# Optimization experiments

Measured on AMD Instinct MI355X. Metric: run time of the kernel, lower is better.

## Reference

```python
import jax, jax.numpy as jnp
import numpy as np

N = 50000      # nodes
E = 640000     # edges
D = 128        # input_dim
O = 128        # output_dim
R = 8          # num_rels


def _uniform(k, shape, fan_in):
    s = 1.0 / np.sqrt(fan_in)
    return jax.random.uniform(k, shape, jnp.float32, -s, s)


def setup_inputs() -> dict:
    key = jax.random.key(0)
    ks = jax.random.split(key, 12)
    x = jax.random.normal(ks[0], (N, D), jnp.float32)
    src = jax.random.randint(ks[1], (E,), 0, N, jnp.int32)
    dst = jax.random.randint(ks[2], (E,), 0, N, jnp.int32)
    etype = jax.random.randint(ks[3], (E,), 0, R, jnp.int32)
    # TypedLinear relation weight bank [R, D, O]
    W_rel = _uniform(ks[4], (R, D, O), D)
    # w1: Linear(D, D)
    w1_W = _uniform(ks[5], (D, D), D)
    w1_b = _uniform(ks[6], (D,), D)
    # MLP (2 layers): Linear(D, O) -> relu -> Linear(O, O)
    m1_W = _uniform(ks[7], (D, O), D)
    m1_b = _uniform(ks[8], (O,), D)
    m2_W = _uniform(ks[9], (O, O), O)
    m2_b = _uniform(ks[10], (O,), O)
    return {"x": x, "src": src, "dst": dst, "etype": etype,
            "W_rel": W_rel, "w1_W": w1_W, "w1_b": w1_b,
            "m1_W": m1_W, "m1_b": m1_b, "m2_W": m2_W, "m2_b": m2_b}


def reference(x, src, dst, etype, W_rel, w1_W, w1_b, m1_W, m1_b, m2_W, m2_b):
    # TypedLinear message: m_e = x[src_e] @ W_rel[etype_e]
    # Since R is small, precompute all relation projections per node [N, R, O]
    # then gather per edge -- avoids materializing per-edge [E, D, O] weights.
    h_all = jnp.einsum('nd,rdo->nro', x, W_rel)          # [N, R, O]
    m = h_all[src, etype]                                 # [E, O] gather
    # scatter-sum aggregation into destination nodes
    agg = jax.ops.segment_sum(m, dst, num_segments=x.shape[0])  # [N, O]
    # update: w1(feat_in) + inneigh, then MLP (linear-relu-linear)
    h = x @ w1_W + w1_b + agg
    h = jax.nn.relu(h @ m1_W + m1_b)
    return h @ m2_W + m2_b
```

## Files before the change

### kernel.cpp

```cpp
#include <hip/hip_runtime.h>
#include <hip/hip_bf16.h>
#include <stdint.h>

#define N_NODES 50000
#define E_EDGES 640000
#define NB_TILES 782
#define NKEY 400000
#define NKEYP 400384
#define SCAN_BLOCKS 391

typedef __attribute__((ext_vector_type(8))) short short8;
typedef __attribute__((ext_vector_type(4))) float float4v;

__device__ __forceinline__ unsigned short f32_to_bf16(float f) {
  uint32_t u = __float_as_uint(f);
  u += 0x7fffu + ((u >> 16) & 1u);
  return (unsigned short)(u >> 16);
}
__device__ __forceinline__ float bf16_to_f32(unsigned short h) {
  return __uint_as_float(((uint32_t)h) << 16);
}

__global__ __launch_bounds__(256) void k_pre(
    const float* __restrict__ x, const float* __restrict__ W_rel,
    const float* __restrict__ w1W, const float* __restrict__ m1W,
    const float* __restrict__ m2W, const int* __restrict__ dst,
    const int* __restrict__ ety,
    unsigned short* __restrict__ xb, unsigned short* __restrict__ wTg,
    int* __restrict__ cnt) {
  int b = blockIdx.x;
  if (b < 6250) {
    int idx = b * 256 + threadIdx.x;
    float4 v = ((const float4*)x)[idx];
    uint32_t p0 = (uint32_t)f32_to_bf16(v.x) | ((uint32_t)f32_to_bf16(v.y) << 16);
    uint32_t p1 = (uint32_t)f32_to_bf16(v.z) | ((uint32_t)f32_to_bf16(v.w) << 16);
    ((uint2*)xb)[idx] = make_uint2(p0, p1);
  } else if (b < 6261) {
    int m = b - 6250;
    const float* srcp = (m < 8) ? (W_rel + (size_t)m * 16384)
                                : (m == 8 ? w1W : (m == 9 ? m1W : m2W));
    unsigned short* dstp = wTg + (size_t)m * 16384;
    for (int i = 0; i < 64; ++i) {
      int idx = threadIdx.x + i * 256;
      int o = idx >> 7, k = idx & 127;
      dstp[idx] = f32_to_bf16(srcp[k * 128 + o]);
    }
  } else {
    int e = (b - 6261) * 256 + threadIdx.x;
    atomicAdd(&cnt[dst[e] * 8 + ety[e]], 1);
  }
}

__global__ __launch_bounds__(1024) void k_scanA(
    const int* __restrict__ cnt, int* __restrict__ off, int* __restrict__ btot) {
  __shared__ int s[1024];
  int t = threadIdx.x, g = blockIdx.x * 1024 + t;
  int v = cnt[g];
  s[t] = v; __syncthreads();
  for (int d = 1; d < 1024; d <<= 1) {
    int a = (t >= d) ? s[t - d] : 0;
    __syncthreads();
    s[t] += a;
    __syncthreads();
  }
  off[g] = s[t] - v;
  if (t == 1023) btot[blockIdx.x] = s[t];
}

__global__ __launch_bounds__(512) void k_scanB(int* __restrict__ btot) {
  __shared__ int s[512];
  int t = threadIdx.x;
  int v = (t < SCAN_BLOCKS) ? btot[t] : 0;
  s[t] = v; __syncthreads();
  for (int d = 1; d < 512; d <<= 1) {
    int a = (t >= d) ? s[t - d] : 0;
    __syncthreads();
    s[t] += a;
    __syncthreads();
  }
  if (t < SCAN_BLOCKS) btot[t] = s[t] - v;
}

__global__ __launch_bounds__(1024) void k_scanC(
    int* __restrict__ off, const int* __restrict__ btot) {
  int g = blockIdx.x * 1024 + threadIdx.x;
  off[g] += btot[blockIdx.x];
}

__global__ __launch_bounds__(256) void k_fill(
    const int* __restrict__ src, const int* __restrict__ dst,
    const int* __restrict__ ety, int* __restrict__ off,
    int* __restrict__ eidx) {
  int e = blockIdx.x * 256 + threadIdx.x;
  if (e >= E_EDGES) return;
  int key = dst[e] * 8 + ety[e];
  int p = atomicAdd(&off[key], 1);
  eidx[p] = src[e];
}

__device__ __forceinline__ void gemm_tile_g(const short (*A)[136],
    const unsigned short* __restrict__ Bt, int wave, int lane, float4v acc[8]) {
  int arow = wave * 16 + (lane & 15);
  int koff = (lane >> 4) * 8;
  #pragma unroll
  for (int kk = 0; kk < 4; ++kk) {
    short8 a = *(const short8*)&A[arow][kk * 32 + koff];
    #pragma unroll
    for (int n = 0; n < 8; ++n) {
      short8 b = *(const short8*)&Bt[(size_t)(n * 16 + (lane & 15)) * 128 + kk * 32 + koff];
      acc[n] = __builtin_amdgcn_mfma_f32_16x16x32_bf16(a, b, acc[n], 0, 0, 0);
    }
  }
}

__global__ __launch_bounds__(256, 4) void k_fused(
    const unsigned short* __restrict__ xb, const unsigned short* __restrict__ wTg,
    const int* __restrict__ off, const int* __restrict__ cnt,
    const int* __restrict__ eidx,
    const float* __restrict__ w1b, const float* __restrict__ m1b,
    const float* __restrict__ m2b, float* __restrict__ out) {
  __shared__ short xs[64][136];
  int tid = threadIdx.x, wave = tid >> 6, lane = tid & 63;
  int q = lane >> 4, l16 = lane & 15;
  int tile0 = blockIdx.x * 64;

  float4v acc[8];
  #pragma unroll
  for (int n = 0; n < 8; ++n) acc[n] = (float4v){0.f, 0.f, 0.f, 0.f};

  for (int r = 0; r < 8; ++r) {
    #pragma unroll
    for (int ri = 0; ri < 4; ++ri) {
      int i = q * 4 + ri;
      int row = wave * 16 + i;
      int key = (tile0 + row) * 8 + r;
      int e1 = off[key], cv = cnt[key];
      float a[8];
      #pragma unroll
      for (int k = 0; k < 8; ++k) a[k] = 0.f;
      int j0 = e1 - cv;
      int sN = (cv > 0) ? eidx[j0] : 0;
      for (int j = j0; j < e1; ++j) {
        int s = sN;
        if (j + 1 < e1) sN = eidx[j + 1];
        short8 w = *(const short8*)&xb[(size_t)s * 128 + l16 * 8];
        #pragma unroll
        for (int k = 0; k < 8; ++k) a[k] += bf16_to_f32((unsigned short)w[k]);
      }
      uint32_t p0 = (uint32_t)f32_to_bf16(a[0]) | ((uint32_t)f32_to_bf16(a[1]) << 16);
      uint32_t p1 = (uint32_t)f32_to_bf16(a[2]) | ((uint32_t)f32_to_bf16(a[3]) << 16);
      uint32_t p2 = (uint32_t)f32_to_bf16(a[4]) | ((uint32_t)f32_to_bf16(a[5]) << 16);
      uint32_t p3 = (uint32_t)f32_to_bf16(a[6]) | ((uint32_t)f32_to_bf16(a[7]) << 16);
      *(uint4*)&xs[row][l16 * 8] = make_uint4(p0, p1, p2, p3);
    }
    gemm_tile_g(xs, wTg + (size_t)r * 16384, wave, lane, acc);
  }

  #pragma unroll
  for (int i = 0; i < 16; ++i) {
    int row = wave * 16 + i;
    int node = tile0 + row;
    uint32_t pv = (node < N_NODES) ? ((const uint32_t*)xb)[(size_t)node * 64 + lane] : 0u;
    *(uint32_t*)&xs[row][lane * 2] = pv;
  }
  gemm_tile_g(xs, wTg + (size_t)8 * 16384, wave, lane, acc);

  #pragma unroll
  for (int n = 0; n < 8; ++n)
    #pragma unroll
    for (int i = 0; i < 4; ++i) {
      int row = wave * 16 + (lane >> 4) * 4 + i;
      int col = n * 16 + (lane & 15);
      xs[row][col] = (short)f32_to_bf16(acc[n][i] + w1b[col]);
    }

  #pragma unroll
  for (int n = 0; n < 8; ++n) acc[n] = (float4v){0.f, 0.f, 0.f, 0.f};
  gemm_tile_g(xs, wTg + (size_t)9 * 16384, wave, lane, acc);
  #pragma unroll
  for (int n = 0; n < 8; ++n)
    #pragma unroll
    for (int i = 0; i < 4; ++i) {
      int row = wave * 16 + (lane >> 4) * 4 + i;
      int col = n * 16 + (lane & 15);
      float v = acc[n][i] + m1b[col];
      xs[row][col] = (short)f32_to_bf16(v > 0.f ? v : 0.f);
    }

  #pragma unroll
  for (int n = 0; n < 8; ++n) acc[n] = (float4v){0.f, 0.f, 0.f, 0.f};
  gemm_tile_g(xs, wTg + (size_t)10 * 16384, wave, lane, acc);
  #pragma unroll
  for (int n = 0; n < 8; ++n)
    #pragma unroll
    for (int i = 0; i < 4; ++i) {
      int row = wave * 16 + (lane >> 4) * 4 + i;
      int col = n * 16 + (lane & 15);
      int node = tile0 + row;
      if (node < N_NODES) out[(size_t)node * 128 + col] = acc[n][i] + m2b[col];
    }
}

extern "C" void kernel_launch(void* const* d_in, const int* in_sizes, int n_in,
                              void* d_out, int out_size, void* d_ws, size_t ws_size,
                              hipStream_t stream) {
  const float* x     = (const float*)d_in[0];
  const int*   src   = (const int*)d_in[1];
  const int*   dst   = (const int*)d_in[2];
  const int*   ety   = (const int*)d_in[3];
  const float* W_rel = (const float*)d_in[4];
  const float* w1W   = (const float*)d_in[5];
  const float* w1b   = (const float*)d_in[6];
  const float* m1W   = (const float*)d_in[7];
  const float* m1b   = (const float*)d_in[8];
  const float* m2W   = (const float*)d_in[9];
  const float* m2b   = (const float*)d_in[10];
  float* out = (float*)d_out;

  char* ws = (char*)d_ws;
  unsigned short* wTg  = (unsigned short*)ws;
  unsigned short* xb   = (unsigned short*)(ws + 524288);
  int*            cnt  = (int*)(ws + 13324288);
  int*            off  = (int*)(ws + 14925824);
  int*            btot = (int*)(ws + 16527360);
  int*            eidx = (int*)(ws + 16531456);

  hipMemsetAsync(cnt, 0, (size_t)NKEYP * 4, stream);
  k_pre<<<8761, 256, 0, stream>>>(x, W_rel, w1W, m1W, m2W, dst, ety, xb, wTg, cnt);
  k_scanA<<<SCAN_BLOCKS, 1024, 0, stream>>>(cnt, off, btot);
  k_scanB<<<1, 512, 0, stream>>>(btot);
  k_scanC<<<SCAN_BLOCKS, 1024, 0, stream>>>(off, btot);
  k_fill<<<E_EDGES / 256, 256, 0, stream>>>(src, dst, ety, off, eidx);
  k_fused<<<NB_TILES, 256, 0, stream>>>(xb, wTg, off, cnt, eidx,
                                        w1b, m1b, m2b, out);
}
```

Measured before the change: 365.9 us.

## Bucket edges by (relation, node tile) and aggregate via LDS atomics

Replaces the per-(node, relation) CSR, which needed 400k keys and a three-kernel scan, with coarse buckets keyed by relation and 64-node tile. The bucket offsets come from a single-block scan, and each edge packs its source index together with its local destination row. In the fused kernel, each wave processes whole edges: it reads a coalesced 256-byte row per edge and accumulates into a float LDS tile with shared-memory atomics. This removes the large counter memset and scan and the per-row loops with divergent lengths, at the cost of LDS atomic contention, an extra 32KB of LDS that lowers occupancy to 3 blocks, and a serial single-block scan.

```diff
diff --git a/kernel.cpp b/kernel.cpp
--- a/kernel.cpp
+++ b/kernel.cpp
@@ -5,9 +5,7 @@
 #define N_NODES 50000
 #define E_EDGES 640000
 #define NB_TILES 782
-#define NKEY 400000
-#define NKEYP 400384
-#define SCAN_BLOCKS 391
+#define NBUCKET 6256
 
 typedef __attribute__((ext_vector_type(8))) short short8;
 typedef __attribute__((ext_vector_type(4))) float float4v;
@@ -16,9 +14,6 @@
   uint32_t u = __float_as_uint(f);
   u += 0x7fffu + ((u >> 16) & 1u);
   return (unsigned short)(u >> 16);
-}
-__device__ __forceinline__ float bf16_to_f32(unsigned short h) {
-  return __uint_as_float(((uint32_t)h) << 16);
 }
 
 __global__ __launch_bounds__(256) void k_pre(
@@ -47,55 +42,45 @@
     }
   } else {
     int e = (b - 6261) * 256 + threadIdx.x;
-    atomicAdd(&cnt[dst[e] * 8 + ety[e]], 1);
-  }
-}
-
-__global__ __launch_bounds__(1024) void k_scanA(
-    const int* __restrict__ cnt, int* __restrict__ off, int* __restrict__ btot) {
+    atomicAdd(&cnt[ety[e] * NB_TILES + (dst[e] >> 6)], 1);
+  }
+}
+
+__global__ __launch_bounds__(1024) void k_scan(
+    const int* __restrict__ cnt, int* __restrict__ offs, int* __restrict__ offcur) {
   __shared__ int s[1024];
-  int t = threadIdx.x, g = blockIdx.x * 1024 + t;
-  int v = cnt[g];
-  s[t] = v; __syncthreads();
-  for (int d = 1; d < 1024; d <<= 1) {
-    int a = (t >= d) ? s[t - d] : 0;
-    __syncthreads();
-    s[t] += a;
-    __syncthreads();
-  }
-  off[g] = s[t] - v;
-  if (t == 1023) btot[blockIdx.x] = s[t];
-}
-
-__global__ __launch_bounds__(512) void k_scanB(int* __restrict__ btot) {
-  __shared__ int s[512];
+  __shared__ int carry;
   int t = threadIdx.x;
-  int v = (t < SCAN_BLOCKS) ? btot[t] : 0;
-  s[t] = v; __syncthreads();
-  for (int d = 1; d < 512; d <<= 1) {
-    int a = (t >= d) ? s[t - d] : 0;
-    __syncthreads();
-    s[t] += a;
-    __syncthreads();
-  }
-  if (t < SCAN_BLOCKS) btot[t] = s[t] - v;
-}
-
-__global__ __launch_bounds__(1024) void k_scanC(
-    int* __restrict__ off, const int* __restrict__ btot) {
-  int g = blockIdx.x * 1024 + threadIdx.x;
-  off[g] += btot[blockIdx.x];
+  if (t == 0) carry = 0;
+  __syncthreads();
+  for (int c = 0; c < 7; ++c) {
+    int g = c * 1024 + t;
+    int v = (g < NBUCKET) ? cnt[g] : 0;
+    s[t] = v;
+    __syncthreads();
+    for (int d = 1; d < 1024; d <<= 1) {
+      int a = (t >= d) ? s[t - d] : 0;
+      __syncthreads();
+      s[t] += a;
+      __syncthreads();
+    }
+    int excl = carry + s[t] - v;
+    if (g <= NBUCKET) { offs[g] = excl; offcur[g] = excl; }
+    __syncthreads();
+    if (t == 1023) carry += s[1023];
+    __syncthreads();
+  }
 }
 
 __global__ __launch_bounds__(256) void k_fill(
     const int* __restrict__ src, const int* __restrict__ dst,
-    const int* __restrict__ ety, int* __restrict__ off,
-    int* __restrict__ eidx) {
+    const int* __restrict__ ety, int* __restrict__ offcur,
+    uint32_t* __restrict__ eidx) {
   int e = blockIdx.x * 256 + threadIdx.x;
   if (e >= E_EDGES) return;
-  int key = dst[e] * 8 + ety[e];
-  int p = atomicAdd(&off[key], 1);
-  eidx[p] = src[e];
+  int b = ety[e] * NB_TILES + (dst[e] >> 6);
+  int p = atomicAdd(&offcur[b], 1);
+  eidx[p] = (uint32_t)src[e] | ((uint32_t)(dst[e] & 63) << 20);
 }
 
 __device__ __forceinline__ void gemm_tile_g(const short (*A)[136],
@@ -113,45 +98,52 @@
   }
 }
 
-__global__ __launch_bounds__(256, 4) void k_fused(
+__global__ __launch_bounds__(256, 3) void k_fused(
     const unsigned short* __restrict__ xb, const unsigned short* __restrict__ wTg,
-    const int* __restrict__ off, const int* __restrict__ cnt,
-    const int* __restrict__ eidx,
+    const int* __restrict__ offs, const uint32_t* __restrict__ eidx,
     const float* __restrict__ w1b, const float* __restrict__ m1b,
     const float* __restrict__ m2b, float* __restrict__ out) {
+  __shared__ float ft[64][128];
   __shared__ short xs[64][136];
   int tid = threadIdx.x, wave = tid >> 6, lane = tid & 63;
-  int q = lane >> 4, l16 = lane & 15;
   int tile0 = blockIdx.x * 64;
+  const uint32_t* xb32 = (const uint32_t*)xb;
 
   float4v acc[8];
   #pragma unroll
   for (int n = 0; n < 8; ++n) acc[n] = (float4v){0.f, 0.f, 0.f, 0.f};
 
+  #pragma unroll
+  for (int i = 0; i < 16; ++i)
+    *(float2*)&ft[wave * 16 + i][lane * 2] = make_float2(0.f, 0.f);
+
   for (int r = 0; r < 8; ++r) {
-    #pragma unroll
-    for (int ri = 0; ri < 4; ++ri) {
-      int i = q * 4 + ri;
+    __syncthreads();
+
+    int bkt = r * NB_TILES + blockIdx.x;
+    int lo = offs[bkt], hi = offs[bkt + 1];
+
+    int e = lo + wave;
+    uint32_t p0 = (e < hi) ? eidx[e] : 0;
+    uint32_t w0 = (e < hi) ? xb32[(size_t)(p0 & 0xFFFFF) * 64 + lane] : 0;
+    uint32_t p1 = (e + 4 < hi) ? eidx[e + 4] : 0;
+    for (; e < hi; e += 4) {
+      uint32_t w1 = (e + 4 < hi) ? xb32[(size_t)(p1 & 0xFFFFF) * 64 + lane] : 0;
+      uint32_t p2 = (e + 8 < hi) ? eidx[e + 8] : 0;
+      int dl = (int)(p0 >> 20);
+      atomicAdd(&ft[dl][lane * 2],     __uint_as_float(w0 << 16));
+      atomicAdd(&ft[dl][lane * 2 + 1], __uint_as_float(w0 & 0xffff0000u));
+      p0 = p1; p1 = p2; w0 = w1;
+    }
+    __syncthreads();
+
+    #pragma unroll
+    for (int i = 0; i < 16; ++i) {
       int row = wave * 16 + i;
-      int key = (tile0 + row) * 8 + r;
-      int e1 = off[key], cv = cnt[key];
-      float a[8];
-      #pragma unroll
-      for (int k = 0; k < 8; ++k) a[k] = 0.f;
-      int j0 = e1 - cv;
-      int sN = (cv > 0) ? eidx[j0] : 0;
-      for (int j = j0; j < e1; ++j) {
-        int s = sN;
-        if (j + 1 < e1) sN = eidx[j + 1];
-        short8 w = *(const short8*)&xb[(size_t)s * 128 + l16 * 8];
-        #pragma unroll
-        for (int k = 0; k < 8; ++k) a[k] += bf16_to_f32((unsigned short)w[k]);
-      }
-      uint32_t p0 = (uint32_t)f32_to_bf16(a[0]) | ((uint32_t)f32_to_bf16(a[1]) << 16);
-      uint32_t p1 = (uint32_t)f32_to_bf16(a[2]) | ((uint32_t)f32_to_bf16(a[3]) << 16);
-      uint32_t p2 = (uint32_t)f32_to_bf16(a[4]) | ((uint32_t)f32_to_bf16(a[5]) << 16);
-      uint32_t p3 = (uint32_t)f32_to_bf16(a[6]) | ((uint32_t)f32_to_bf16(a[7]) << 16);
-      *(uint4*)&xs[row][l16 * 8] = make_uint4(p0, p1, p2, p3);
+      float2 f = *(const float2*)&ft[row][lane * 2];
+      *(float2*)&ft[row][lane * 2] = make_float2(0.f, 0.f);
+      uint32_t pk = (uint32_t)f32_to_bf16(f.x) | ((uint32_t)f32_to_bf16(f.y) << 16);
+      *(uint32_t*)&xs[row][lane * 2] = pk;
     }
     gemm_tile_g(xs, wTg + (size_t)r * 16384, wave, lane, acc);
   }
@@ -160,7 +152,7 @@
   for (int i = 0; i < 16; ++i) {
     int row = wave * 16 + i;
     int node = tile0 + row;
-    uint32_t pv = (node < N_NODES) ? ((const uint32_t*)xb)[(size_t)node * 64 + lane] : 0u;
+    uint32_t pv = (node < N_NODES) ? xb32[(size_t)node * 64 + lane] : 0u;
     *(uint32_t*)&xs[row][lane * 2] = pv;
   }
   gemm_tile_g(xs, wTg + (size_t)8 * 16384, wave, lane, acc);
@@ -218,19 +210,16 @@
   float* out = (float*)d_out;
 
   char* ws = (char*)d_ws;
-  unsigned short* wTg  = (unsigned short*)ws;
-  unsigned short* xb   = (unsigned short*)(ws + 524288);
-  int*            cnt  = (int*)(ws + 13324288);
-  int*            off  = (int*)(ws + 14925824);
-  int*            btot = (int*)(ws + 16527360);
-  int*            eidx = (int*)(ws + 16531456);
-
-  hipMemsetAsync(cnt, 0, (size_t)NKEYP * 4, stream);
+  unsigned short* wTg    = (unsigned short*)ws;
+  unsigned short* xb     = (unsigned short*)(ws + 524288);
+  int*            cnt    = (int*)(ws + 13324288);
+  int*            offs   = (int*)(ws + 13357056);
+  int*            offcur = (int*)(ws + 13389824);
+  uint32_t*       eidx   = (uint32_t*)(ws + 13422592);
+
+  hipMemsetAsync(cnt, 0, (size_t)NBUCKET * 4, stream);
   k_pre<<<8761, 256, 0, stream>>>(x, W_rel, w1W, m1W, m2W, dst, ety, xb, wTg, cnt);
-  k_scanA<<<SCAN_BLOCKS, 1024, 0, stream>>>(cnt, off, btot);
-  k_scanB<<<1, 512, 0, stream>>>(btot);
-  k_scanC<<<SCAN_BLOCKS, 1024, 0, stream>>>(off, btot);
-  k_fill<<<E_EDGES / 256, 256, 0, stream>>>(src, dst, ety, off, eidx);
-  k_fused<<<NB_TILES, 256, 0, stream>>>(xb, wTg, off, cnt, eidx,
-                                        w1b, m1b, m2b, out);
-}
+  k_scan<<<1, 1024, 0, stream>>>(cnt, offs, offcur);
+  k_fill<<<E_EDGES / 256, 256, 0, stream>>>(src, dst, ety, offcur, eidx);
+  k_fused<<<NB_TILES, 256, 0, stream>>>(xb, wTg, offs, eidx, w1b, m1b, m2b, out);
+}
```

After: 805.3 us. 2.2x slower.
